# Optimization experiments

Measured on AMD Instinct MI355X. Metric: run time of the kernel, lower is better.

The kernel has to match this reference:

```python
import jax, jax.numpy as jnp
import numpy as np

EMB = 256
HID = 1024
N_TRACKS = 4096
SEQ = 9
SCALE = 4.0


def setup_inputs() -> dict:
    key = jax.random.key(0)
    ks = jax.random.split(key, 12)

    def init(k, shape, fan_in):
        b = 1.0 / np.sqrt(fan_in)
        return jax.random.uniform(k, shape, jnp.float32, -b, b)

    return {
        "observed": jax.random.normal(ks[0], (SEQ, N_TRACKS, 2), jnp.float32),
        "emb_w": init(ks[1], (EMB - 2, 2), 2),
        "emb_b": init(ks[2], (EMB - 2,), 2),
        "enc_wih": init(ks[3], (4 * HID, EMB), HID),
        "enc_whh": init(ks[4], (4 * HID, HID), HID),
        "enc_b": init(ks[5], (4 * HID,), HID),
        "dec_wih": init(ks[6], (4 * HID, EMB), HID),
        "dec_whh": init(ks[7], (4 * HID, HID), HID),
        "dec_b": init(ks[8], (4 * HID,), HID),
        "h2n_w": init(ks[9], (5, HID), HID),
        "h2n_b": init(ks[10], (5,), HID),
        "n_predict": 12,
    }


def _forward(observed, emb_w, emb_b, enc_wih, enc_whh, enc_b,
             dec_wih, dec_whh, dec_b, h2n_w, h2n_b, n_predict):
    n = observed.shape[1]
    H = enc_whh.shape[1]
    E = enc_wih.shape[1]

    def cell(x, h, c, wih, whh, b):
        # PyTorch LSTMCell gate order: i, f, g, o
        g = x @ wih.T + h @ whh.T + b
        i, f, gg, o = jnp.split(g, 4, axis=-1)
        c = jax.nn.sigmoid(f) * c + jax.nn.sigmoid(i) * jnp.tanh(gg)
        h = jax.nn.sigmoid(o) * jnp.tanh(c)
        return h, c

    def embed(v):
        # Linear(2, E-2) -> ReLU, then 2 zero tag channels
        e = jax.nn.relu((v * SCALE) @ emb_w.T + emb_b)
        return jnp.concatenate([e, jnp.zeros((v.shape[0], 2), e.dtype)], axis=1)

    def h2n(h):
        raw = h @ h2n_w.T + h2n_b
        sig = 0.01 + 0.2 * jax.nn.sigmoid(raw[:, 2:4])  # sigma1, sigma2
        rho = 0.7 * jax.nn.sigmoid(raw[:, 4:5])          # rho
        return jnp.concatenate([raw[:, :2], sig, rho], axis=1)

    def step(params, h, c, obs1, obs2):
        wih, whh, b = params
        mask = ~(jnp.isnan(obs1[:, 0]) | jnp.isnan(obs2[:, 0]))  # [N]
        x = embed(obs2 - obs1)
        h2, c2 = cell(x, h, c, wih, whh, b)
        nrm = h2n(h2)
        m = mask[:, None]
        h = jnp.where(m, h2, h)
        c = jnp.where(m, c2, c)
        normal = jnp.where(m, nrm, jnp.nan)
        pos = obs2 + normal[:, :2]
        return h, c, normal, pos

    h = jnp.zeros((n, H), observed.dtype)
    c = jnp.zeros((n, H), observed.dtype)

    # encoder start tag
    tag_enc = jnp.zeros((n, E), observed.dtype).at[:, -2].set(1.0)
    h, c = cell(tag_enc, h, c, enc_wih, enc_whh, enc_b)

    enc_p = (enc_wih, enc_whh, enc_b)

    def enc_scan(carry, obs_pair):
        h, c = carry
        o1, o2 = obs_pair
        h, c, normal, pos = step(enc_p, h, c, o1, o2)
        return (h, c), (normal, pos)

    (h, c), (enc_normals, enc_positions) = jax.lax.scan(
        enc_scan, (h, c), (observed[:-1], observed[1:]))

    # decoder start tag
    tag_dec = jnp.zeros((n, E), observed.dtype).at[:, -1].set(1.0)
    h, c = cell(tag_dec, h, c, dec_wih, dec_whh, dec_b)

    dec_p = (dec_wih, dec_whh, dec_b)
    p1, p2 = enc_positions[-2], enc_positions[-1]

    def dec_scan(carry, _):
        h, c, p1, p2 = carry
        o1 = jax.lax.stop_gradient(p1)  # .detach() in torch
        o2 = jax.lax.stop_gradient(p2)
        h, c, normal, pos = step(dec_p, h, c, o1, o2)
        return (h, c, p2, pos), (normal, pos)

    _, (dec_normals, dec_positions) = jax.lax.scan(
        dec_scan, (h, c, p1, p2), None, length=n_predict - 1)

    rel_pred_scene = jnp.concatenate([enc_normals, dec_normals], axis=0)
    pred_scene = jnp.concatenate([enc_positions, dec_positions], axis=0)
    return rel_pred_scene, pred_scene


def reference(observed, emb_w, emb_b, enc_wih, enc_whh, enc_b,
              dec_wih, dec_whh, dec_b, h2n_w, h2n_b, n_predict):
    return _forward(observed, emb_w, emb_b, enc_wih, enc_whh, enc_b,
                    dec_wih, dec_whh, dec_b, h2n_w, h2n_b, n_predict)
```

## Files before the change

kernel.cpp:

```cpp
#include <hip/hip_runtime.h>
#include <stdint.h>

#define NTRK 4096
#define HIDN 1024
#define EMBN 256
#define KTOT 1280
#define NOUT 19

typedef __attribute__((ext_vector_type(8))) short short8;
typedef __attribute__((ext_vector_type(4))) float f32x4;

typedef __attribute__((address_space(1))) const void GV;
typedef __attribute__((address_space(3))) void LV;

__device__ __forceinline__ uint16_t f2bf(float f) {
  uint32_t u = __float_as_uint(f);
  u += 0x7fffu + ((u >> 16) & 1u);
  return (uint16_t)(u >> 16);
}
__device__ __forceinline__ float bf2f(uint16_t v) {
  return __uint_as_float(((uint32_t)v) << 16);
}
__device__ __forceinline__ float sigm(float x) { return 1.0f / (1.0f + expf(-x)); }
__device__ __forceinline__ float sigmf_(float x) {
  return __builtin_amdgcn_rcpf(1.0f + __expf(-x));
}
__device__ __forceinline__ float tanhf_(float x) {
  return 2.0f * __builtin_amdgcn_rcpf(1.0f + __expf(-2.0f * x)) - 1.0f;
}

__global__ __launch_bounds__(256) void prep_weights(
    const float* __restrict__ encWih, const float* __restrict__ encWhh,
    const float* __restrict__ encB,
    const float* __restrict__ decWih, const float* __restrict__ decWhh,
    const float* __restrict__ decB,
    uint16_t* __restrict__ WcatE, uint16_t* __restrict__ WcatD,
    float* __restrict__ biasE, float* __restrict__ biasD, float* __restrict__ biasDT)
{
  const int jp = blockIdx.x;
  const int q = jp >> 6, r = jp & 63;
  const int gate = r >> 4, l16 = r & 15;
  const int u = q * 16 + l16;
  const int orig = gate * 1024 + u;
  const int t = threadIdx.x;

  WcatE[(size_t)jp * KTOT + t] = f2bf(encWih[(size_t)orig * 256 + t]);
  WcatD[(size_t)jp * KTOT + t] = f2bf(decWih[(size_t)orig * 256 + t]);
#pragma unroll
  for (int c = 0; c < 4; c++) {
    WcatE[(size_t)jp * KTOT + 256 + c * 256 + t] = f2bf(encWhh[(size_t)orig * 1024 + c * 256 + t]);
    WcatD[(size_t)jp * KTOT + 256 + c * 256 + t] = f2bf(decWhh[(size_t)orig * 1024 + c * 256 + t]);
  }
  if (t == 0) {
    biasE[jp]  = encB[orig];
    biasD[jp]  = decB[orig];
    biasDT[jp] = decB[orig] + decWih[(size_t)orig * 256 + 255];
  }
}

__global__ void init_h0(const float* __restrict__ encWih, const float* __restrict__ encB,
                        float* __restrict__ h0, float* __restrict__ c0)
{
  const int u = blockIdx.x * 256 + threadIdx.x;
  if (u >= 1024) return;
  const float gi = encWih[(size_t)(u) * 256 + 254]        + encB[u];
  const float gg = encWih[(size_t)(2048 + u) * 256 + 254] + encB[2048 + u];
  const float go = encWih[(size_t)(3072 + u) * 256 + 254] + encB[3072 + u];
  const float c = sigm(gi) * tanhf(gg);
  c0[u] = c;
  h0[u] = sigm(go) * tanhf(c);
}

__global__ __launch_bounds__(256) void bias_h0(
    const float* __restrict__ encWhh, const float* __restrict__ encB,
    const float* __restrict__ h0, float* __restrict__ biasE0)
{
  const int jp = blockIdx.x * 4 + (threadIdx.x >> 6);
  const int lane = threadIdx.x & 63;
  const int q = jp >> 6, r = jp & 63;
  const int gate = r >> 4, l16 = r & 15;
  const int orig = gate * 1024 + (q * 16 + l16);
  const float* wr = encWhh + (size_t)orig * 1024 + lane * 16;
  const float* hr = h0 + lane * 16;
  float s = 0.f;
#pragma unroll
  for (int e = 0; e < 16; e++) s += wr[e] * hr[e];
  s += __shfl_xor(s, 32); s += __shfl_xor(s, 16); s += __shfl_xor(s, 8);
  s += __shfl_xor(s, 4);  s += __shfl_xor(s, 2);  s += __shfl_xor(s, 1);
  if (lane == 0) biasE0[jp] = encB[orig] + s;
}

__global__ void fill_state(const float* __restrict__ h0, const float* __restrict__ c0,
                           uint16_t* __restrict__ H, float* __restrict__ Cst)
{
  const size_t i = (size_t)blockIdx.x * 256 + threadIdx.x;
  const int u = (int)(i & 1023);
  H[i] = f2bf(h0[u]);
  Cst[i] = c0[u];
}

__global__ __launch_bounds__(256) void embed_k(
    const float* __restrict__ o1, const float* __restrict__ o2,
    const float* __restrict__ ew, const float* __restrict__ eb,
    uint16_t* __restrict__ X)
{
  const int trk = blockIdx.x;
  const int j = threadIdx.x;
  const float vx = (o2[trk * 2]     - o1[trk * 2])     * 4.0f;
  const float vy = (o2[trk * 2 + 1] - o1[trk * 2 + 1]) * 4.0f;
  float e = 0.f;
  if (j < 254) e = fmaxf(vx * ew[j * 2] + vy * ew[j * 2 + 1] + eb[j], 0.f);
  X[(size_t)trk * 256 + j] = f2bf(e);
}

__global__ __launch_bounds__(256) void embed8(
    const float* __restrict__ observed, const float* __restrict__ ew,
    const float* __restrict__ eb, uint16_t* __restrict__ Xall)
{
  const int t = blockIdx.y;
  const int trk = blockIdx.x;
  const int j = threadIdx.x;
  const float* o1 = observed + ((size_t)t * 4096 + trk) * 2;
  const float* o2 = o1 + 4096 * 2;
  const float vx = (o2[0] - o1[0]) * 4.0f;
  const float vy = (o2[1] - o1[1]) * 4.0f;
  float e = 0.f;
  if (j < 254) e = fmaxf(vx * ew[j * 2] + vy * ew[j * 2 + 1] + eb[j], 0.f);
  Xall[((size_t)t * 4096 + trk) * 256 + j] = f2bf(e);
}

__global__ __launch_bounds__(512, 4) void gemm_lstm(
    const uint16_t* __restrict__ X,    const uint16_t* __restrict__ Hin,
    const uint16_t* __restrict__ Wcat, const float* __restrict__ bias,
    float* __restrict__ Cst,           uint16_t* __restrict__ Hout,
    const float* __restrict__ obs1,    const float* __restrict__ obs2,
    int k0, int kend, int maskmode)
{
  __shared__ uint16_t As[3 * 4096];
  __shared__ uint16_t Bs[3 * 8192];
  __shared__ uint8_t  smask[128];

  const int tid  = threadIdx.x;
  const int w    = tid >> 6;
  const int lane = tid & 63;
  const int wr   = w >> 2;
  const int wc   = w & 3;
  const int quad = lane >> 4;
  const int l15  = lane & 15;

  const int bid = blockIdx.y * 16 + blockIdx.x;
  const int xcd = bid & 7;
  const int j   = bid >> 3;
  const int bmS = (xcd >> 2) * 16 + (j >> 2);
  const int bnS = (xcd & 3) * 4 + (j & 3);
  const int bm  = bmS * 128;
  const int bn  = bnS * 256;

  const int NT = (kend - k0) >> 5;

  if (tid < 128) {
    bool m = true;
    if (maskmode) {
      const float a = obs1[(bm + tid) * 2];
      const float b = obs2[(bm + tid) * 2];
      m = !((a != a) || (b != b));
    }
    smask[tid] = m ? 1 : 0;
  }

  const int srow = w * 16 + (lane >> 2);
  const int sch  = ((lane & 3) ^ ((lane >> 3) & 3)) * 8;
  const uint16_t* pXr = X ? X + (size_t)(bm + srow) * 256 + sch : (const uint16_t*)0;
  const uint16_t* pHr = Hin  + (size_t)(bm + srow) * 1024 + sch;
  const uint16_t* pWr = Wcat + (size_t)(bn + srow) * (size_t)KTOT + sch;

  auto stage = [&](int V, int slot) {
    if (V >= NT) return;
    const int kg = k0 + V * 32;
    uint16_t* ad = As + slot * 4096 + w * 16 * 32;
    if (kg < 256) {
      __builtin_amdgcn_global_load_lds((GV*)(pXr + kg),         (LV*)ad, 16, 0, 0);
    } else {
      __builtin_amdgcn_global_load_lds((GV*)(pHr + (kg - 256)), (LV*)ad, 16, 0, 0);
    }
    uint16_t* bd = Bs + slot * 8192 + w * 16 * 32;
    __builtin_amdgcn_global_load_lds((GV*)(pWr + kg),                        (LV*)bd,          16, 0, 0);
    __builtin_amdgcn_global_load_lds((GV*)(pWr + (size_t)128 * KTOT + kg),   (LV*)(bd + 4096), 16, 0, 0);
  };

  f32x4 acc[4][4];
#pragma unroll
  for (int i = 0; i < 4; i++)
#pragma unroll
    for (int n = 0; n < 4; n++) acc[i][n] = (f32x4){0.f, 0.f, 0.f, 0.f};

  stage(0, 0); stage(1, 1);
  asm volatile("s_waitcnt vmcnt(3)" ::: "memory");
  __builtin_amdgcn_s_barrier();

  const int cc = (quad ^ ((l15 >> 1) & 3)) * 8;

  int sT = 0;
  for (int T = 0; T < NT; T++) {
    const int sS = (sT == 0) ? 2 : sT - 1;
    const uint16_t* Ab = As + sT * 4096;
    const uint16_t* Bb = Bs + sT * 8192;
    short8 a[4], b[4];
#pragma unroll
    for (int i = 0; i < 4; i++)
      a[i] = *(const short8*)(Ab + (wr * 64 + i * 16 + l15) * 32 + cc);
#pragma unroll
    for (int n = 0; n < 4; n++)
      b[n] = *(const short8*)(Bb + (wc * 64 + n * 16 + l15) * 32 + cc);
    stage(T + 2, sS);
    __builtin_amdgcn_s_setprio(1);
#pragma unroll
    for (int i = 0; i < 4; i++)
#pragma unroll
      for (int n = 0; n < 4; n++)
        acc[i][n] = __builtin_amdgcn_mfma_f32_16x16x32_bf16(a[i], b[n], acc[i][n], 0, 0, 0);
    __builtin_amdgcn_s_setprio(0);
    if (T < NT - 2) {
      asm volatile("s_waitcnt vmcnt(3)" ::: "memory");
    } else {
      asm volatile("s_waitcnt vmcnt(0)" ::: "memory");
    }
    __builtin_amdgcn_s_barrier();
    sT = (sT == 2) ? 0 : sT + 1;
  }

  const int u  = ((bn >> 6) + wc) * 16 + l15;
  const int jb = bn + wc * 64 + l15;
  const float b_i = bias[jb];
  const float b_f = bias[jb + 16];
  const float b_g = bias[jb + 32];
  const float b_o = bias[jb + 48];

#pragma unroll
  for (int i = 0; i < 4; i++) {
#pragma unroll
    for (int r = 0; r < 4; r++) {
      const int row = bm + wr * 64 + i * 16 + quad * 4 + r;
      const size_t idx = (size_t)row * 1024 + u;
      uint16_t hv;
      if (smask[row - bm]) {
        const float gi = acc[i][0][r] + b_i;
        const float gf = acc[i][1][r] + b_f;
        const float gg = acc[i][2][r] + b_g;
        const float go = acc[i][3][r] + b_o;
        const float cn = sigmf_(gf) * Cst[idx] + sigmf_(gi) * tanhf_(gg);
        Cst[idx] = cn;
        hv = f2bf(sigmf_(go) * tanhf_(cn));
      } else {
        hv = Hin[idx];
      }
      Hout[idx] = hv;
    }
  }
}

__global__ __launch_bounds__(256) void h2n_pos(
    const uint16_t* __restrict__ H, const float* __restrict__ w5, const float* __restrict__ b5,
    const float* __restrict__ obs1, const float* __restrict__ obs2,
    float* __restrict__ outrel, float* __restrict__ outpos,
    const float* __restrict__ pprev, const float* __restrict__ ew,
    const float* __restrict__ eb, uint16_t* __restrict__ Xnext, int do_embed)
{
  const int lane  = threadIdx.x & 63;
  const int track = blockIdx.x * 4 + (threadIdx.x >> 6);

  const uint16_t* hrow = H + (size_t)track * 1024 + lane * 16;
  const short8 v0 = *(const short8*)(hrow);
  const short8 v1 = *(const short8*)(hrow + 8);
  float hv[16];
#pragma unroll
  for (int j = 0; j < 8; j++) {
    hv[j]     = bf2f((uint16_t)v0[j]);
    hv[8 + j] = bf2f((uint16_t)v1[j]);
  }
  const int kb = lane * 16;
  float p[5];
#pragma unroll
  for (int o = 0; o < 5; o++) {
    const float* wr = w5 + (size_t)o * 1024 + kb;
    float s = 0.f;
#pragma unroll
    for (int j = 0; j < 16; j++) s += hv[j] * wr[j];
    p[o] = s;
  }
#pragma unroll
  for (int o = 0; o < 5; o++) {
    float v = p[o];
    v += __shfl_xor(v, 32); v += __shfl_xor(v, 16); v += __shfl_xor(v, 8);
    v += __shfl_xor(v, 4);  v += __shfl_xor(v, 2);  v += __shfl_xor(v, 1);
    p[o] = v;
  }
  const float o1x = obs1[track * 2];
  const float o2x = obs2[track * 2];
  const float o2y = obs2[track * 2 + 1];
  const bool msk = !((o1x != o1x) || (o2x != o2x));
  float n0 = p[0] + b5[0];
  float n1 = p[1] + b5[1];
  float n2 = 0.01f + 0.2f * sigmf_(p[2] + b5[2]);
  float n3 = 0.01f + 0.2f * sigmf_(p[3] + b5[3]);
  float n4 = 0.7f  * sigmf_(p[4] + b5[4]);
  if (!msk) {
    const float qn = __uint_as_float(0x7fc00000u);
    n0 = n1 = n2 = n3 = n4 = qn;
  }
  const float posx = o2x + n0;
  const float posy = o2y + n1;
  if (lane == 0) {
    float* rr = outrel + (size_t)track * 5;
    rr[0] = n0; rr[1] = n1; rr[2] = n2; rr[3] = n3; rr[4] = n4;
    outpos[track * 2]     = posx;
    outpos[track * 2 + 1] = posy;
  }
  if (do_embed) {
    const float vx = (posx - pprev[track * 2])     * 4.0f;
    const float vy = (posy - pprev[track * 2 + 1]) * 4.0f;
    uint16_t* xr = Xnext + (size_t)track * 256;
#pragma unroll
    for (int ii = 0; ii < 4; ii++) {
      const int j = ii * 64 + lane;
      float e = 0.f;
      if (j < 254) e = fmaxf(vx * ew[j * 2] + vy * ew[j * 2 + 1] + eb[j], 0.f);
      xr[j] = f2bf(e);
    }
  }
}

extern "C" void kernel_launch(void* const* d_in, const int* in_sizes, int n_in,
                              void* d_out, int out_size, void* d_ws, size_t ws_size,
                              hipStream_t stream)
{
  const float* observed = (const float*)d_in[0];
  const float* emb_w    = (const float*)d_in[1];
  const float* emb_b    = (const float*)d_in[2];
  const float* enc_wih  = (const float*)d_in[3];
  const float* enc_whh  = (const float*)d_in[4];
  const float* enc_b    = (const float*)d_in[5];
  const float* dec_wih  = (const float*)d_in[6];
  const float* dec_whh  = (const float*)d_in[7];
  const float* dec_b    = (const float*)d_in[8];
  const float* h2n_w    = (const float*)d_in[9];
  const float* h2n_b    = (const float*)d_in[10];

  char* ws = (char*)d_ws;
  size_t off = 0;
  auto alloc = [&](size_t bytes) -> void* {
    size_t cur = (off + 255) & ~(size_t)255;
    off = cur + bytes;
    return (void*)(ws + cur);
  };
  uint16_t* WcatE = (uint16_t*)alloc((size_t)4096 * KTOT * 2);
  uint16_t* WcatD = (uint16_t*)alloc((size_t)4096 * KTOT * 2);
  float*    biasE = (float*)alloc(4096 * 4);
  float*    biasE0= (float*)alloc(4096 * 4);
  float*    biasD = (float*)alloc(4096 * 4);
  float*    biasDT= (float*)alloc(4096 * 4);
  float*    h0    = (float*)alloc(1024 * 4);
  float*    c0    = (float*)alloc(1024 * 4);
  uint16_t* HA    = (uint16_t*)alloc((size_t)4096 * 1024 * 2);
  uint16_t* HB    = (uint16_t*)alloc((size_t)4096 * 1024 * 2);
  float*    Cst   = (float*)alloc((size_t)4096 * 1024 * 4);
  uint16_t* Xb    = (uint16_t*)alloc((size_t)4096 * 256 * 2);
  const size_t xall_bytes = (size_t)8 * 4096 * 256 * 2;
  const bool use_xall = (off + 256 + xall_bytes) <= ws_size;
  uint16_t* Xall = use_xall ? (uint16_t*)alloc(xall_bytes) : nullptr;

  float* outrel = (float*)d_out;
  float* outpos = outrel + (size_t)NOUT * 4096 * 5;

  prep_weights<<<4096, 256, 0, stream>>>(enc_wih, enc_whh, enc_b, dec_wih, dec_whh, dec_b,
                                         WcatE, WcatD, biasE, biasD, biasDT);
  init_h0<<<4, 256, 0, stream>>>(enc_wih, enc_b, h0, c0);
  bias_h0<<<1024, 256, 0, stream>>>(enc_whh, enc_b, h0, biasE0);
  fill_state<<<16384, 256, 0, stream>>>(h0, c0, HA, Cst);
  if (use_xall) {
    embed8<<<dim3(4096, 8), 256, 0, stream>>>(observed, emb_w, emb_b, Xall);
  }

  uint16_t* Hin = HA;
  uint16_t* Hout = HB;
  const dim3 ggrid(16, 32);

  for (int t = 0; t < 8; t++) {
    const float* o1 = observed + (size_t)t * 4096 * 2;
    const float* o2 = observed + (size_t)(t + 1) * 4096 * 2;
    uint16_t* Xt = Xb;
    if (use_xall) {
      Xt = Xall + (size_t)t * 4096 * 256;
    } else {
      embed_k<<<4096, 256, 0, stream>>>(o1, o2, emb_w, emb_b, Xb);
    }
    if (t == 0) {
      gemm_lstm<<<ggrid, 512, 0, stream>>>(Xt, Hin, WcatE, biasE0, Cst, Hout, o1, o2, 0, 256, 1);
    } else {
      gemm_lstm<<<ggrid, 512, 0, stream>>>(Xt, Hin, WcatE, biasE, Cst, Hout, o1, o2, 0, KTOT, 1);
    }
    const int de = (t == 7) ? 1 : 0;
    h2n_pos<<<1024, 256, 0, stream>>>(Hout, h2n_w, h2n_b, o1, o2,
                                      outrel + (size_t)t * 4096 * 5,
                                      outpos + (size_t)t * 4096 * 2,
                                      outpos + (size_t)6 * 4096 * 2, emb_w, emb_b, Xb, de);
    uint16_t* tmp = Hin; Hin = Hout; Hout = tmp;
  }

  gemm_lstm<<<ggrid, 512, 0, stream>>>(nullptr, Hin, WcatD, biasDT, Cst, Hout,
                                       nullptr, nullptr, 256, KTOT, 0);
  { uint16_t* tmp = Hin; Hin = Hout; Hout = tmp; }

  for (int s = 0; s < 11; s++) {
    const float* p1 = outpos + (size_t)(6 + s) * 4096 * 2;
    const float* p2 = outpos + (size_t)(7 + s) * 4096 * 2;
    gemm_lstm<<<ggrid, 512, 0, stream>>>(Xb, Hin, WcatD, biasD, Cst, Hout, p1, p2, 0, KTOT, 1);
    const int de = (s < 10) ? 1 : 0;
    h2n_pos<<<1024, 256, 0, stream>>>(Hout, h2n_w, h2n_b, p1, p2,
                                      outrel + (size_t)(8 + s) * 4096 * 5,
                                      outpos + (size_t)(8 + s) * 4096 * 2,
                                      p2, emb_w, emb_b, Xb, de);
    uint16_t* tmp = Hin; Hin = Hout; Hout = tmp;
  }
}
```

Measured before the change: 1.231 ms.

## Deepen GEMM LDS pipeline to four stages with register double-buffered fragments

Moves the fused LSTM GEMM from a 3-slot LDS ring to a 4-slot ring with three tiles prefetched. The main loop is unrolled by two and ping-pongs two register fragment sets, so the LDS reads for the next tile overlap the MFMAs on the current one. The goal is to hide global and LDS latency behind compute. The cost is more LDS (96KB tiles) and more registers, so launch bounds drop from 4 to 2 blocks per CU, which lowers occupancy.

```diff
diff --git a/kernel.cpp b/kernel.cpp
--- a/kernel.cpp
+++ b/kernel.cpp
@@ -129,15 +129,15 @@
   Xall[((size_t)t * 4096 + trk) * 256 + j] = f2bf(e);
 }
 
-__global__ __launch_bounds__(512, 4) void gemm_lstm(
+__global__ __launch_bounds__(512, 2) void gemm_lstm(
     const uint16_t* __restrict__ X,    const uint16_t* __restrict__ Hin,
     const uint16_t* __restrict__ Wcat, const float* __restrict__ bias,
     float* __restrict__ Cst,           uint16_t* __restrict__ Hout,
     const float* __restrict__ obs1,    const float* __restrict__ obs2,
     int k0, int kend, int maskmode)
 {
-  __shared__ uint16_t As[3 * 4096];
-  __shared__ uint16_t Bs[3 * 8192];
+  __shared__ uint16_t As[4 * 4096];
+  __shared__ uint16_t Bs[4 * 8192];
   __shared__ uint8_t  smask[128];
 
   const int tid  = threadIdx.x;
@@ -174,9 +174,10 @@
   const uint16_t* pHr = Hin  + (size_t)(bm + srow) * 1024 + sch;
   const uint16_t* pWr = Wcat + (size_t)(bn + srow) * (size_t)KTOT + sch;
 
-  auto stage = [&](int V, int slot) {
+  auto stage = [&](int V) {
     if (V >= NT) return;
     const int kg = k0 + V * 32;
+    const int slot = V & 3;
     uint16_t* ad = As + slot * 4096 + w * 16 * 32;
     if (kg < 256) {
       __builtin_amdgcn_global_load_lds((GV*)(pXr + kg),         (LV*)ad, 16, 0, 0);
@@ -188,31 +189,26 @@
     __builtin_amdgcn_global_load_lds((GV*)(pWr + (size_t)128 * KTOT + kg),   (LV*)(bd + 4096), 16, 0, 0);
   };
 
-  f32x4 acc[4][4];
-#pragma unroll
-  for (int i = 0; i < 4; i++)
-#pragma unroll
-    for (int n = 0; n < 4; n++) acc[i][n] = (f32x4){0.f, 0.f, 0.f, 0.f};
-
-  stage(0, 0); stage(1, 1);
-  asm volatile("s_waitcnt vmcnt(3)" ::: "memory");
-  __builtin_amdgcn_s_barrier();
-
   const int cc = (quad ^ ((l15 >> 1) & 3)) * 8;
 
-  int sT = 0;
-  for (int T = 0; T < NT; T++) {
-    const int sS = (sT == 0) ? 2 : sT - 1;
-    const uint16_t* Ab = As + sT * 4096;
-    const uint16_t* Bb = Bs + sT * 8192;
-    short8 a[4], b[4];
+  auto rdfrag = [&](int V, short8 (&a)[4], short8 (&b)[4]) {
+    const uint16_t* Ab = As + (V & 3) * 4096;
+    const uint16_t* Bb = Bs + (V & 3) * 8192;
 #pragma unroll
     for (int i = 0; i < 4; i++)
       a[i] = *(const short8*)(Ab + (wr * 64 + i * 16 + l15) * 32 + cc);
 #pragma unroll
     for (int n = 0; n < 4; n++)
       b[n] = *(const short8*)(Bb + (wc * 64 + n * 16 + l15) * 32 + cc);
-    stage(T + 2, sS);
+  };
+
+  f32x4 acc[4][4];
+#pragma unroll
+  for (int i = 0; i < 4; i++)
+#pragma unroll
+    for (int n = 0; n < 4; n++) acc[i][n] = (f32x4){0.f, 0.f, 0.f, 0.f};
+
+  auto mfma16 = [&](short8 (&a)[4], short8 (&b)[4]) {
     __builtin_amdgcn_s_setprio(1);
 #pragma unroll
     for (int i = 0; i < 4; i++)
@@ -220,13 +216,35 @@
       for (int n = 0; n < 4; n++)
         acc[i][n] = __builtin_amdgcn_mfma_f32_16x16x32_bf16(a[i], b[n], acc[i][n], 0, 0, 0);
     __builtin_amdgcn_s_setprio(0);
-    if (T < NT - 2) {
+  };
+
+  short8 a0[4], b0[4], a1[4], b1[4];
+
+  stage(0); stage(1); stage(2);
+  asm volatile("s_waitcnt vmcnt(3)" ::: "memory");
+  __builtin_amdgcn_s_barrier();
+  rdfrag(0, a0, b0);
+
+  for (int T = 0; T < NT; T += 2) {
+    stage(T + 3);
+    if (T + 1 < NT) rdfrag(T + 1, a1, b1);
+    mfma16(a0, b0);
+    if (T < NT - 3) {
       asm volatile("s_waitcnt vmcnt(3)" ::: "memory");
     } else {
       asm volatile("s_waitcnt vmcnt(0)" ::: "memory");
     }
     __builtin_amdgcn_s_barrier();
-    sT = (sT == 2) ? 0 : sT + 1;
+
+    stage(T + 4);
+    if (T + 2 < NT) rdfrag(T + 2, a0, b0);
+    mfma16(a1, b1);
+    if (T + 1 < NT - 3) {
+      asm volatile("s_waitcnt vmcnt(3)" ::: "memory");
+    } else {
+      asm volatile("s_waitcnt vmcnt(0)" ::: "memory");
+    }
+    __builtin_amdgcn_s_barrier();
   }
 
   const int u  = ((bn >> 6) + wc) * 16 + l15;
```

After: 1.844 ms. 49.8% more time.
